# Kernel optimization log

Measured on AMD Instinct MI355X. Metric: run time of the kernel, lower is better.

Reference implementation:

```python
import jax, jax.numpy as jnp
import numpy as np

B, H, F = 4096, 32, 1024     # batch, hp_num, feat_dim
N_CAT, CAT_DIM = 8, 16       # categorical dims 0..7, each |domain| = 16
N_CONT = H - N_CAT
LN_EPS = 1e-5


def setup_inputs() -> dict:
    key = jax.random.key(0)
    ks = jax.random.split(key, 8)
    s = 1.0 / np.sqrt(F)  # ~xavier scale
    return {
        "z": jax.random.normal(ks[0], (B, F), jnp.float32),
        "edge": jax.random.randint(ks[1], (2, 10), 0, B),
        # stacked per-hp projection Linears (weights stored as [in, out])
        "W_proj": jax.random.normal(ks[2], (H, F, F), jnp.float32) * s,
        "b_proj": jnp.zeros((H, F), jnp.float32),
        # LayerNorm over [hp_num, feat_dim]
        "ln_w": jnp.ones((H, F), jnp.float32),
        "ln_b": jnp.zeros((H, F), jnp.float32),
        # reverse_embedding for categorical dims (softmax heads)
        "W_cat": jax.random.normal(ks[3], (N_CAT, F, CAT_DIM), jnp.float32) * s,
        "b_cat": jnp.zeros((N_CAT, CAT_DIM), jnp.float32),
        # reverse_embedding for continuous dims (scalar heads)
        "W_cont": jax.random.normal(ks[4], (N_CONT, F, 1), jnp.float32) * s,
        "b_cont": jnp.zeros((N_CONT, 1), jnp.float32),
    }


def reference(z, edge, W_proj, b_proj, ln_w, ln_b, W_cat, b_cat, W_cont, b_cont):
    # per-hp projection: batched GEMM replacing batch*hp_num tiny Linears
    latent = jnp.einsum('bf,hfd->bhd', z, W_proj) + b_proj  # [B, H, F]
    # LayerNorm normalized over the last two dims [hp_num, feat_dim]
    mu = latent.mean(axis=(1, 2), keepdims=True)
    var = latent.var(axis=(1, 2), keepdims=True)
    latent = (latent - mu) * jax.lax.rsqrt(var + LN_EPS) * ln_w + ln_b
    latent = jax.nn.relu(latent)
    # reverse embeddings: categorical heads (dims 0..N_CAT-1) get softmax
    cat_logits = jnp.einsum('bhf,hfc->bhc', latent[:, :N_CAT], W_cat) + b_cat
    pred_cat = jax.nn.softmax(cat_logits, axis=-1)          # [B, N_CAT, CAT_DIM]
    pred_cont = jnp.einsum('bhf,hfc->bhc', latent[:, N_CAT:], W_cont) + b_cont  # [B, N_CONT, 1]
    return pred_cat, pred_cont, latent
```

## Files before the change

kernel.cpp:

```cpp
#include <hip/hip_runtime.h>

typedef unsigned short u16;
typedef unsigned int u32;
typedef __bf16 bf16x8 __attribute__((ext_vector_type(8)));
typedef float f32x4 __attribute__((ext_vector_type(4)));

#define B_SZ   4096
#define H_NUM  32
#define F_DIM  1024
#define NTOT   (H_NUM * F_DIM)
#define N_CAT  8
#define CAT_D  16
#define N_CONT 24
#define LN_EPS 1e-5f
#define NSTRIP 128

__device__ __forceinline__ u16 f2bf(float f) {
    unsigned int u = __builtin_bit_cast(unsigned int, f);
    unsigned int r = (u + 0x7FFFu + ((u >> 16) & 1u)) >> 16;
    return (u16)r;
}

__device__ __forceinline__ float bf2f(u16 v) {
    unsigned int u = ((unsigned int)v) << 16;
    return __builtin_bit_cast(float, u);
}

__device__ __forceinline__ float bflo(u32 v) { return bf2f((u16)(v & 0xffffu)); }
__device__ __forceinline__ float bfhi(u32 v) { return bf2f((u16)(v >> 16)); }

__device__ __forceinline__ void gl2lds16(const void* g, void* l) {
    __builtin_amdgcn_global_load_lds(
        (const __attribute__((address_space(1))) void*)g,
        (__attribute__((address_space(3))) void*)l,
        16, 0, 0);
}

__device__ __forceinline__ float wave_sum(float v) {
#pragma unroll
    for (int o = 32; o; o >>= 1) v += __shfl_xor(v, o);
    return v;
}

__global__ __launch_bounds__(256) void zconv(const float* __restrict__ z,
                                             u16* __restrict__ zb) {
    int i = blockIdx.x * 256 + threadIdx.x;
    float4 v = ((const float4*)z)[i];
    ushort4 o;
    o.x = f2bf(v.x); o.y = f2bf(v.y); o.z = f2bf(v.z); o.w = f2bf(v.w);
    ((ushort4*)zb)[i] = o;
}

__global__ __launch_bounds__(256) void packln(const float* __restrict__ lnw,
                                              const float* __restrict__ lnb,
                                              const float* __restrict__ wcont,
                                              uint4* __restrict__ lnwb,
                                              ushort4* __restrict__ wc16) {
    int idx = blockIdx.x * 256 + threadIdx.x;
    if (idx < NTOT / 4) {
        float4 w = ((const float4*)lnw)[idx];
        float4 b = ((const float4*)lnb)[idx];
        uint4 o;
        o.x = (u32)f2bf(w.x) | ((u32)f2bf(w.y) << 16);
        o.y = (u32)f2bf(w.z) | ((u32)f2bf(w.w) << 16);
        o.z = (u32)f2bf(b.x) | ((u32)f2bf(b.y) << 16);
        o.w = (u32)f2bf(b.z) | ((u32)f2bf(b.w) << 16);
        lnwb[idx] = o;
    } else if (idx < NTOT / 4 + N_CONT * F_DIM / 4) {
        int j = idx - NTOT / 4;
        float4 v = ((const float4*)wcont)[j];
        ushort4 o;
        o.x = f2bf(v.x); o.y = f2bf(v.y); o.z = f2bf(v.z); o.w = f2bf(v.w);
        wc16[j] = o;
    }
}

__global__ __launch_bounds__(256) void transpose_w(const float* __restrict__ W,
                                                   u16* __restrict__ Wt) {
    __shared__ u16 tile[64][72];
    const int h = blockIdx.z;
    const int f0 = blockIdx.x * 64;
    const int d0 = blockIdx.y * 64;
    const float* Wh = W + (size_t)h * F_DIM * F_DIM;
    u16* Wth = Wt + (size_t)h * F_DIM * F_DIM;
    const int t = threadIdx.x;

#pragma unroll
    for (int i = 0; i < 4; ++i) {
        int idx = i * 256 + t;
        int fr = idx >> 4;
        int c4 = idx & 15;
        float4 v = *(const float4*)(Wh + (size_t)(f0 + fr) * F_DIM + d0 + c4 * 4);
        tile[fr][c4 * 4 + 0] = f2bf(v.x);
        tile[fr][c4 * 4 + 1] = f2bf(v.y);
        tile[fr][c4 * 4 + 2] = f2bf(v.z);
        tile[fr][c4 * 4 + 3] = f2bf(v.w);
    }
    __syncthreads();
#pragma unroll
    for (int i = 0; i < 2; ++i) {
        int idx = i * 256 + t;
        int dr = idx >> 3;
        int c8 = idx & 7;
        __attribute__((aligned(16))) u16 tmp[8];
#pragma unroll
        for (int j = 0; j < 8; ++j) tmp[j] = tile[c8 * 8 + j][dr];
        *(uint4*)(Wth + (size_t)(d0 + dr) * F_DIM + f0 + c8 * 8) = *(const uint4*)tmp;
    }
}

template <int BF>
__global__ __launch_bounds__(512, 2) void gemm256(const u16* __restrict__ A,
                                                  const u16* __restrict__ Bt,
                                                  const float* __restrict__ bproj,
                                                  u16* __restrict__ lat16,
                                                  float* __restrict__ latf,
                                                  float* __restrict__ psum,
                                                  float* __restrict__ psumsq) {
    extern __shared__ u16 dynlds[];
    const int t = threadIdx.x;
    const int wid = t >> 6;
    const int lane = t & 63;
    const int l16 = lane & 15;
    const int lk = lane >> 4;
    const int wm = wid >> 2;
    const int wn = wid & 3;

    const int wg = blockIdx.x;
    const int xcd = wg & 7;
    const int local = wg >> 3;
    const int m0 = (local & 15) * 256;
    const int n0 = ((xcd << 4) + (local >> 4)) * 256;

    f32x4 acc[8][4];
    const f32x4 zero = {0.f, 0.f, 0.f, 0.f};
#pragma unroll
    for (int m = 0; m < 8; ++m)
#pragma unroll
        for (int n = 0; n < 4; ++n) acc[m][n] = zero;

    auto stage = [&](int p, int ktn, int bn) {
        const char* srcbase = (p < 2) ? (const char*)A : (const char*)Bt;
        const int rowbase = (p < 2) ? (m0 + p * 128) : (n0 + (p - 2) * 128);
        u16* ldsbase = dynlds + bn * 32768 + (p >> 1) * 16384 + (p & 1) * 8192;
#pragma unroll
        for (int i = 0; i < 2; ++i) {
            int oo = i * 8192 + t * 16;
            int oos = oo ^ (((oo >> 7) & 7) << 4);
            int row = oo >> 7;
            int colb = oos & 127;
            gl2lds16(srcbase + (size_t)(rowbase + row) * 2048 + ktn * 128 + colb,
                     ldsbase + i * 4096 + (wid << 9));
        }
    };

#pragma unroll
    for (int p = 0; p < 4; ++p) stage(p, 0, 0);
    __syncthreads();

    const int swz = (l16 & 7) << 4;
    for (int kt = 0; kt < 16; ++kt) {
        const int buf = kt & 1;
        const char* aB = (const char*)(dynlds + buf * 32768 + wm * 8192);
        const char* bB = (const char*)(dynlds + buf * 32768 + 16384 + (wn >> 1) * 8192);

        if (kt < 15) {
#pragma unroll
            for (int p = 0; p < 4; ++p) stage(p, kt + 1, buf ^ 1);
        }

        bf16x8 bfr[4][2];
#pragma unroll
        for (int p = 0; p < 4; ++p) {
            if (p == 0) {
#pragma unroll
                for (int nr = 0; nr < 4; ++nr)
#pragma unroll
                    for (int kk = 0; kk < 2; ++kk)
                        bfr[nr][kk] = *(const bf16x8*)(bB +
                            ((wn & 1) * 64 + nr * 16 + l16) * 128 +
                            ((kk * 64 + lk * 16) ^ swz));
            }
            bf16x8 afr[2][2];
#pragma unroll
            for (int mr = 0; mr < 2; ++mr)
#pragma unroll
                for (int kk = 0; kk < 2; ++kk)
                    afr[mr][kk] = *(const bf16x8*)(aB +
                        (p * 32 + mr * 16 + l16) * 128 +
                        ((kk * 64 + lk * 16) ^ swz));
            __builtin_amdgcn_s_setprio(1);
#pragma unroll
            for (int kk = 0; kk < 2; ++kk)
#pragma unroll
                for (int mr = 0; mr < 2; ++mr)
#pragma unroll
                    for (int nr = 0; nr < 4; ++nr)
                        acc[p * 2 + mr][nr] = __builtin_amdgcn_mfma_f32_16x16x32_bf16(
                            afr[mr][kk], bfr[nr][kk], acc[p * 2 + mr][nr], 0, 0, 0);
            __builtin_amdgcn_s_setprio(0);
        }
        __syncthreads();
    }

    float bias[4];
#pragma unroll
    for (int nr = 0; nr < 4; ++nr) bias[nr] = bproj[n0 + wn * 64 + nr * 16 + l16];

    float sm[8][4], s2[8][4];
#pragma unroll
    for (int mr = 0; mr < 8; ++mr)
#pragma unroll
        for (int j = 0; j < 4; ++j) { sm[mr][j] = 0.f; s2[mr][j] = 0.f; }

#pragma unroll
    for (int mr = 0; mr < 8; ++mr) {
#pragma unroll
        for (int j = 0; j < 4; ++j) {
            const int rowg = m0 + wm * 128 + mr * 16 + lk * 4 + j;
            size_t off = (size_t)rowg * NTOT + n0 + wn * 64 + l16;
#pragma unroll
            for (int nr = 0; nr < 4; ++nr) {
                float v = acc[mr][nr][j] + bias[nr];
                if (BF) lat16[off + nr * 16] = f2bf(v);
                else    latf[off + nr * 16] = v;
                sm[mr][j] += v;
                s2[mr][j] += v * v;
            }
        }
    }
#pragma unroll
    for (int o = 1; o < 16; o <<= 1) {
#pragma unroll
        for (int mr = 0; mr < 8; ++mr)
#pragma unroll
            for (int j = 0; j < 4; ++j) {
                sm[mr][j] += __shfl_xor(sm[mr][j], o);
                s2[mr][j] += __shfl_xor(s2[mr][j], o);
            }
    }
    float* sredf = (float*)dynlds;
    float* s2f   = sredf + 1024;
    __syncthreads();
    if (l16 == 0) {
#pragma unroll
        for (int mr = 0; mr < 8; ++mr)
#pragma unroll
            for (int j = 0; j < 4; ++j) {
                int r = wm * 128 + mr * 16 + lk * 4 + j;
                sredf[wn * 256 + r] = sm[mr][j];
                s2f[wn * 256 + r] = s2[mr][j];
            }
    }
    __syncthreads();
    if (t < 256) {
        const int strip = n0 >> 8;
        float S = sredf[t] + sredf[256 + t] + sredf[512 + t] + sredf[768 + t];
        float S2 = s2f[t] + s2f[256 + t] + s2f[512 + t] + s2f[768 + t];
        psum[(size_t)strip * B_SZ + m0 + t] = S;
        psumsq[(size_t)strip * B_SZ + m0 + t] = S2;
    }
}

__global__ __launch_bounds__(256) void ln_finalize(const float* __restrict__ psum,
                                                   const float* __restrict__ psumsq,
                                                   float* __restrict__ murs) {
    const int t = threadIdx.x;
    const int b0 = blockIdx.x * 64;
    const int tb = t & 63;
    const int tg = t >> 6;
    float s = 0.f, s2 = 0.f;
    for (int sidx = tg; sidx < NSTRIP; sidx += 4) {
        s += psum[(size_t)sidx * B_SZ + b0 + tb];
        s2 += psumsq[(size_t)sidx * B_SZ + b0 + tb];
    }
    __shared__ float r1[4][64], r2[4][64];
    r1[tg][tb] = s;
    r2[tg][tb] = s2;
    __syncthreads();
    if (t < 64) {
        float S = r1[0][t] + r1[1][t] + r1[2][t] + r1[3][t];
        float S2 = r2[0][t] + r2[1][t] + r2[2][t] + r2[3][t];
        float m = S / (float)NTOT;
        float var = S2 / (float)NTOT - m * m;
        murs[b0 + t] = m;
        murs[B_SZ + b0 + t] = rsqrtf(var + LN_EPS);
    }
}

template <int BF>
__global__ __launch_bounds__(256) void headsJ(const void* __restrict__ latin_,
                                              float* __restrict__ latout,
                                              const float* __restrict__ murs,
                                              const uint4* __restrict__ lnwb,
                                              const ushort4* __restrict__ wc16,
                                              const float* __restrict__ Wcat,
                                              const float* __restrict__ bcat,
                                              const float* __restrict__ bcont,
                                              float* __restrict__ pcat,
                                              float* __restrict__ pcont) {
    const int b = blockIdx.x;
    const int t = threadIdx.x;
    const int lane = t & 63;
    const int w4 = t >> 6;
    const float mu = murs[b];
    const float rs = murs[B_SZ + b];
    const ushort4* lin16 = (const ushort4*)((const u16*)latin_ + (size_t)b * NTOT);
    const float4*  linf  = (const float4*)((const float*)latin_ + (size_t)b * NTOT);
    float4* lout4 = (float4*)(latout + (size_t)b * NTOT);

    __shared__ ushort4 sy16[N_CAT * 256];
    __shared__ float4 cred4[4][N_CAT][4];
    __shared__ float nred[N_CONT][4];

    float cp[N_CONT];

#pragma unroll 2
    for (int k = 0; k < N_CAT; ++k) {
        const int i = (k << 8) + t;
        float4 x;
        if (BF) {
            ushort4 xv = lin16[i];
            x.x = bf2f(xv.x); x.y = bf2f(xv.y); x.z = bf2f(xv.z); x.w = bf2f(xv.w);
        } else {
            x = linf[i];
        }
        uint4 wb = lnwb[i];
        float4 yo;
        yo.x = fmaxf(0.f, (x.x - mu) * rs * bflo(wb.x) + bflo(wb.z));
        yo.y = fmaxf(0.f, (x.y - mu) * rs * bfhi(wb.x) + bfhi(wb.z));
        yo.z = fmaxf(0.f, (x.z - mu) * rs * bflo(wb.y) + bflo(wb.w));
        yo.w = fmaxf(0.f, (x.w - mu) * rs * bfhi(wb.y) + bfhi(wb.w));
        lout4[i] = yo;
        ushort4 ys;
        ys.x = f2bf(yo.x); ys.y = f2bf(yo.y); ys.z = f2bf(yo.z); ys.w = f2bf(yo.w);
        sy16[i] = ys;
    }

#pragma unroll 2
    for (int k = N_CAT; k < H_NUM; ++k) {
        const int i = (k << 8) + t;
        float4 x;
        if (BF) {
            ushort4 xv = lin16[i];
            x.x = bf2f(xv.x); x.y = bf2f(xv.y); x.z = bf2f(xv.z); x.w = bf2f(xv.w);
        } else {
            x = linf[i];
        }
        uint4 wb = lnwb[i];
        ushort4 wv = wc16[((k - N_CAT) << 8) + t];
        float4 yo;
        yo.x = fmaxf(0.f, (x.x - mu) * rs * bflo(wb.x) + bflo(wb.z));
        yo.y = fmaxf(0.f, (x.y - mu) * rs * bfhi(wb.x) + bfhi(wb.z));
        yo.z = fmaxf(0.f, (x.z - mu) * rs * bflo(wb.y) + bflo(wb.w));
        yo.w = fmaxf(0.f, (x.w - mu) * rs * bfhi(wb.y) + bfhi(wb.w));
        lout4[i] = yo;
        cp[k - N_CAT] = yo.x * bf2f(wv.x) + yo.y * bf2f(wv.y) +
                        yo.z * bf2f(wv.z) + yo.w * bf2f(wv.w);
    }
    __syncthreads();

    const int cq = t & 3;
    const int fg = t >> 2;
    for (int k = 0; k < N_CAT; ++k) {
        const float4* Wc4 = (const float4*)(Wcat + (size_t)k * F_DIM * CAT_D);
        float4 a4 = {0.f, 0.f, 0.f, 0.f};
#pragma unroll
        for (int jq = 0; jq < 4; ++jq) {
            ushort4 yv = sy16[(k << 8) + fg * 4 + jq];
            float ys[4] = {bf2f(yv.x), bf2f(yv.y), bf2f(yv.z), bf2f(yv.w)};
#pragma unroll
            for (int r = 0; r < 4; ++r) {
                int f = fg * 16 + jq * 4 + r;
                float4 wv = Wc4[f * 4 + cq];
                a4.x += ys[r] * wv.x;
                a4.y += ys[r] * wv.y;
                a4.z += ys[r] * wv.z;
                a4.w += ys[r] * wv.w;
            }
        }
#pragma unroll
        for (int o = 4; o < 64; o <<= 1) {
            a4.x += __shfl_xor(a4.x, o);
            a4.y += __shfl_xor(a4.y, o);
            a4.z += __shfl_xor(a4.z, o);
            a4.w += __shfl_xor(a4.w, o);
        }
        if (lane < 4) cred4[w4][k][lane] = a4;
    }
#pragma unroll
    for (int k = 0; k < N_CONT; ++k) {
        float v = wave_sum(cp[k]);
        if (lane == 0) nred[k][w4] = v;
    }
    __syncthreads();

    if (t < 128) {
        const int h = t >> 4, c = t & 15;
        float lg = bcat[h * CAT_D + c];
#pragma unroll
        for (int w = 0; w < 4; ++w)
            lg += ((const float*)cred4[w][h])[c];
        float mx = lg;
#pragma unroll
        for (int o = 8; o; o >>= 1) mx = fmaxf(mx, __shfl_xor(mx, o, 16));
        float e = __expf(lg - mx);
        float sm2 = e;
#pragma unroll
        for (int o = 8; o; o >>= 1) sm2 += __shfl_xor(sm2, o, 16);
        pcat[(size_t)b * (N_CAT * CAT_D) + t] = e / sm2;
    } else if (t >= 128 && t < 128 + N_CONT) {
        const int ci = t - 128;
        pcont[(size_t)b * N_CONT + ci] =
            nred[ci][0] + nred[ci][1] + nred[ci][2] + nred[ci][3] + bcont[ci];
    }
}

extern "C" void kernel_launch(void* const* d_in, const int* in_sizes, int n_in,
                              void* d_out, int out_size, void* d_ws, size_t ws_size,
                              hipStream_t stream) {
    const float* z     = (const float*)d_in[0];
    const float* Wp    = (const float*)d_in[2];
    const float* bp    = (const float*)d_in[3];
    const float* lnw   = (const float*)d_in[4];
    const float* lnb   = (const float*)d_in[5];
    const float* Wcat  = (const float*)d_in[6];
    const float* bcat  = (const float*)d_in[7];
    const float* Wcont = (const float*)d_in[8];
    const float* bcont = (const float*)d_in[9];

    float* out    = (float*)d_out;
    float* pcat   = out;
    float* pcont  = out + (size_t)B_SZ * N_CAT * CAT_D;
    float* latent = pcont + (size_t)B_SZ * N_CONT;

    u16* zb     = (u16*)d_ws;
    u16* Wt     = zb + (size_t)B_SZ * F_DIM;
    float* murs = (float*)(Wt + (size_t)NTOT * F_DIM);
    float* psum   = murs + 2 * B_SZ;
    float* psumsq = psum + (size_t)B_SZ * NSTRIP;
    uint4* lnwb = (uint4*)(psumsq + (size_t)B_SZ * NSTRIP);
    ushort4* wc16 = (ushort4*)(lnwb + NTOT / 4);
    u16* lat16  = (u16*)(wc16 + N_CONT * F_DIM / 4);

    const size_t need = (size_t)((char*)(lat16 + (size_t)B_SZ * NTOT) - (char*)d_ws);
    const bool usebf = ws_size >= need;

    const int LDSB = 131072;
    zconv<<<dim3(B_SZ * F_DIM / 1024), 256, 0, stream>>>(z, zb);
    packln<<<dim3((NTOT / 4 + N_CONT * F_DIM / 4 + 255) / 256), 256, 0, stream>>>(
        lnw, lnb, Wcont, lnwb, wc16);
    transpose_w<<<dim3(16, 16, 32), 256, 0, stream>>>(Wp, Wt);
    if (usebf) {
        (void)hipFuncSetAttribute((const void*)gemm256<1>,
                                  hipFuncAttributeMaxDynamicSharedMemorySize, LDSB);
        gemm256<1><<<dim3(2048), 512, LDSB, stream>>>(zb, Wt, bp, lat16, nullptr,
                                                      psum, psumsq);
        ln_finalize<<<dim3(B_SZ / 64), 256, 0, stream>>>(psum, psumsq, murs);
        headsJ<1><<<dim3(B_SZ), 256, 0, stream>>>(lat16, latent, murs, lnwb, wc16,
                                                  Wcat, bcat, bcont, pcat, pcont);
    } else {
        (void)hipFuncSetAttribute((const void*)gemm256<0>,
                                  hipFuncAttributeMaxDynamicSharedMemorySize, LDSB);
        gemm256<0><<<dim3(2048), 512, LDSB, stream>>>(zb, Wt, bp, nullptr, latent,
                                                      psum, psumsq);
        ln_finalize<<<dim3(B_SZ / 64), 256, 0, stream>>>(psum, psumsq, murs);
        headsJ<0><<<dim3(B_SZ), 256, 0, stream>>>(latent, latent, murs, lnwb, wc16,
                                                  Wcat, bcat, bcont, pcat, pcont);
    }
}
```

Before: 698.6 us.

## Split heads kernel into separate continuous and categorical kernels

Replaces the single per-row heads kernel with two kernels. A continuous-head kernel runs over a (3, B) grid, with each block handling 8 of the 24 continuous hp slices. A categorical kernel handles the 8 softmax slices per row. This spreads the memory-bound LayerNorm/ReLU/writeback work across more, lighter blocks, which lowers register pressure (24 partial sums down to 8) and raises parallelism. The cost is an extra launch and repeated reads of the per-row mean and rstd.

```diff
diff --git a/kernel.cpp b/kernel.cpp
--- a/kernel.cpp
+++ b/kernel.cpp
@@ -289,16 +289,70 @@
 }
 
 template <int BF>
-__global__ __launch_bounds__(256) void headsJ(const void* __restrict__ latin_,
-                                              float* __restrict__ latout,
-                                              const float* __restrict__ murs,
-                                              const uint4* __restrict__ lnwb,
-                                              const ushort4* __restrict__ wc16,
-                                              const float* __restrict__ Wcat,
-                                              const float* __restrict__ bcat,
-                                              const float* __restrict__ bcont,
-                                              float* __restrict__ pcat,
-                                              float* __restrict__ pcont) {
+__global__ __launch_bounds__(256) void contK(const void* __restrict__ latin_,
+                                             float* __restrict__ latout,
+                                             const float* __restrict__ murs,
+                                             const uint4* __restrict__ lnwb,
+                                             const ushort4* __restrict__ wc16,
+                                             const float* __restrict__ bcont,
+                                             float* __restrict__ pcont) {
+    const int g = blockIdx.x;
+    const int b = blockIdx.y;
+    const int t = threadIdx.x;
+    const int lane = t & 63;
+    const int w4 = t >> 6;
+    const float mu = murs[b];
+    const float rs = murs[B_SZ + b];
+    const ushort4* lin16 = (const ushort4*)((const u16*)latin_ + (size_t)b * NTOT);
+    const float4*  linf  = (const float4*)((const float*)latin_ + (size_t)b * NTOT);
+    float4* lout4 = (float4*)(latout + (size_t)b * NTOT);
+
+    __shared__ float red[8][4];
+
+    float cp8[8];
+#pragma unroll
+    for (int j = 0; j < 8; ++j) {
+        const int k = N_CAT + g * 8 + j;
+        const int i = (k << 8) + t;
+        float4 x;
+        if (BF) {
+            ushort4 xv = lin16[i];
+            x.x = bf2f(xv.x); x.y = bf2f(xv.y); x.z = bf2f(xv.z); x.w = bf2f(xv.w);
+        } else {
+            x = linf[i];
+        }
+        uint4 wb = lnwb[i];
+        ushort4 wv = wc16[((g * 8 + j) << 8) + t];
+        float4 yo;
+        yo.x = fmaxf(0.f, (x.x - mu) * rs * bflo(wb.x) + bflo(wb.z));
+        yo.y = fmaxf(0.f, (x.y - mu) * rs * bfhi(wb.x) + bfhi(wb.z));
+        yo.z = fmaxf(0.f, (x.z - mu) * rs * bflo(wb.y) + bflo(wb.w));
+        yo.w = fmaxf(0.f, (x.w - mu) * rs * bfhi(wb.y) + bfhi(wb.w));
+        lout4[i] = yo;
+        cp8[j] = yo.x * bf2f(wv.x) + yo.y * bf2f(wv.y) +
+                 yo.z * bf2f(wv.z) + yo.w * bf2f(wv.w);
+    }
+#pragma unroll
+    for (int j = 0; j < 8; ++j) {
+        float v = wave_sum(cp8[j]);
+        if (lane == 0) red[j][w4] = v;
+    }
+    __syncthreads();
+    if (t < 8) {
+        const int ci = g * 8 + t;
+        pcont[(size_t)b * N_CONT + ci] =
+            red[t][0] + red[t][1] + red[t][2] + red[t][3] + bcont[ci];
+    }
+}
+
+template <int BF>
+__global__ __launch_bounds__(256) void catK(const void* __restrict__ latin_,
+                                            float* __restrict__ latout,
+                                            const float* __restrict__ murs,
+                                            const uint4* __restrict__ lnwb,
+                                            const float* __restrict__ Wcat,
+                                            const float* __restrict__ bcat,
+                                            float* __restrict__ pcat) {
     const int b = blockIdx.x;
     const int t = threadIdx.x;
     const int lane = t & 63;
@@ -311,11 +365,8 @@
 
     __shared__ ushort4 sy16[N_CAT * 256];
     __shared__ float4 cred4[4][N_CAT][4];
-    __shared__ float nred[N_CONT][4];
-
-    float cp[N_CONT];
-
-#pragma unroll 2
+
+#pragma unroll
     for (int k = 0; k < N_CAT; ++k) {
         const int i = (k << 8) + t;
         float4 x;
@@ -336,28 +387,6 @@
         ys.x = f2bf(yo.x); ys.y = f2bf(yo.y); ys.z = f2bf(yo.z); ys.w = f2bf(yo.w);
         sy16[i] = ys;
     }
-
-#pragma unroll 2
-    for (int k = N_CAT; k < H_NUM; ++k) {
-        const int i = (k << 8) + t;
-        float4 x;
-        if (BF) {
-            ushort4 xv = lin16[i];
-            x.x = bf2f(xv.x); x.y = bf2f(xv.y); x.z = bf2f(xv.z); x.w = bf2f(xv.w);
-        } else {
-            x = linf[i];
-        }
-        uint4 wb = lnwb[i];
-        ushort4 wv = wc16[((k - N_CAT) << 8) + t];
-        float4 yo;
-        yo.x = fmaxf(0.f, (x.x - mu) * rs * bflo(wb.x) + bflo(wb.z));
-        yo.y = fmaxf(0.f, (x.y - mu) * rs * bfhi(wb.x) + bfhi(wb.z));
-        yo.z = fmaxf(0.f, (x.z - mu) * rs * bflo(wb.y) + bflo(wb.w));
-        yo.w = fmaxf(0.f, (x.w - mu) * rs * bfhi(wb.y) + bfhi(wb.w));
-        lout4[i] = yo;
-        cp[k - N_CAT] = yo.x * bf2f(wv.x) + yo.y * bf2f(wv.y) +
-                        yo.z * bf2f(wv.z) + yo.w * bf2f(wv.w);
-    }
     __syncthreads();
 
     const int cq = t & 3;
@@ -388,11 +417,6 @@
         }
         if (lane < 4) cred4[w4][k][lane] = a4;
     }
-#pragma unroll
-    for (int k = 0; k < N_CONT; ++k) {
-        float v = wave_sum(cp[k]);
-        if (lane == 0) nred[k][w4] = v;
-    }
     __syncthreads();
 
     if (t < 128) {
@@ -409,10 +433,6 @@
 #pragma unroll
         for (int o = 8; o; o >>= 1) sm2 += __shfl_xor(sm2, o, 16);
         pcat[(size_t)b * (N_CAT * CAT_D) + t] = e / sm2;
-    } else if (t >= 128 && t < 128 + N_CONT) {
-        const int ci = t - 128;
-        pcont[(size_t)b * N_CONT + ci] =
-            nred[ci][0] + nred[ci][1] + nred[ci][2] + nred[ci][3] + bcont[ci];
     }
 }
 
@@ -457,15 +477,19 @@
         gemm256<1><<<dim3(2048), 512, LDSB, stream>>>(zb, Wt, bp, lat16, nullptr,
                                                       psum, psumsq);
         ln_finalize<<<dim3(B_SZ / 64), 256, 0, stream>>>(psum, psumsq, murs);
-        headsJ<1><<<dim3(B_SZ), 256, 0, stream>>>(lat16, latent, murs, lnwb, wc16,
-                                                  Wcat, bcat, bcont, pcat, pcont);
+        contK<1><<<dim3(3, B_SZ), 256, 0, stream>>>(lat16, latent, murs, lnwb, wc16,
+                                                    bcont, pcont);
+        catK<1><<<dim3(B_SZ), 256, 0, stream>>>(lat16, latent, murs, lnwb,
+                                                Wcat, bcat, pcat);
     } else {
         (void)hipFuncSetAttribute((const void*)gemm256<0>,
                                   hipFuncAttributeMaxDynamicSharedMemorySize, LDSB);
         gemm256<0><<<dim3(2048), 512, LDSB, stream>>>(zb, Wt, bp, nullptr, latent,
                                                       psum, psumsq);
         ln_finalize<<<dim3(B_SZ / 64), 256, 0, stream>>>(psum, psumsq, murs);
-        headsJ<0><<<dim3(B_SZ), 256, 0, stream>>>(latent, latent, murs, lnwb, wc16,
-                                                  Wcat, bcat, bcont, pcat, pcont);
-    }
-}
+        contK<0><<<dim3(3, B_SZ), 256, 0, stream>>>(latent, latent, murs, lnwb, wc16,
+                                                    bcont, pcont);
+        catK<0><<<dim3(B_SZ), 256, 0, stream>>>(latent, latent, murs, lnwb,
+                                                Wcat, bcat, pcat);
+    }
+}
```

Measured after the change: 661.7 us. 5.3% less time.
